# Kernel optimization log

Measured on AMD Instinct MI355X. Metric: run time of the kernel, lower is better.

Reference implementation:

```python
import jax, jax.numpy as jnp
import numpy as np

BN_EPS = 1e-5

def gin_layer(x, src, dst, w1, b1, w2, b2, gamma, beta):
    # GINConv with eps=0: h_i = MLP(x_i + sum_{j->i} x_j)
    agg = jax.ops.segment_sum(x[src], dst, num_segments=x.shape[0])  # [N, D]
    h = x + agg
    h = jnp.maximum(h @ w1 + b1, 0.0) @ w2 + b2
    # BatchNorm (training-mode batch statistics, biased var as in torch)
    mu = jnp.mean(h, axis=0)
    var = jnp.var(h, axis=0)
    h = (h - mu) * jax.lax.rsqrt(var + BN_EPS) * gamma + beta
    return jnp.maximum(h, 0.0)  # ReLU (dropout = identity in eval)

def setup_inputs() -> dict:
    key = jax.random.key(0)
    N, E, G = 20000, 320000, 64
    dims = [128, 128, 256, 512]
    ks = jax.random.split(key, 32)
    inp = {
        "x": jax.random.normal(ks[0], (N, dims[0]), dtype=jnp.float32),
        "edge_index": jax.random.randint(ks[1], (2, E), 0, N, dtype=jnp.int64),
        "batch_idx": jnp.sort(jax.random.randint(ks[2], (N,), 0, G, dtype=jnp.int64)),
    }
    ki = 3
    for li, (di, do) in enumerate(zip(dims[:-1], dims[1:])):
        s = chr(ord('a') + li)
        inp[f"w1{s}"] = jax.random.normal(ks[ki], (di, do), dtype=jnp.float32) * (1.0 / np.sqrt(di)); ki += 1
        inp[f"b1{s}"] = jnp.zeros((do,), dtype=jnp.float32)
        inp[f"w2{s}"] = jax.random.normal(ks[ki], (do, do), dtype=jnp.float32) * (1.0 / np.sqrt(do)); ki += 1
        inp[f"b2{s}"] = jnp.zeros((do,), dtype=jnp.float32)
        inp[f"gn{s}"] = jnp.ones((do,), dtype=jnp.float32)
        inp[f"bn{s}"] = jnp.zeros((do,), dtype=jnp.float32)
    inp["wo"] = jax.random.normal(ks[ki], (dims[-1], 64), dtype=jnp.float32) * (1.0 / np.sqrt(dims[-1]))
    inp["bo"] = jnp.zeros((64,), dtype=jnp.float32)
    return inp

def reference(x, edge_index, batch_idx,
              w1a, b1a, w2a, b2a, gna, bna,
              w1b, b1b, w2b, b2b, gnb, bnb,
              w1c, b1c, w2c, b2c, gnc, bnc,
              wo, bo):
    G = 64
    src, dst = edge_index[0], edge_index[1]
    h = gin_layer(x, src, dst, w1a, b1a, w2a, b2a, gna, bna)
    h = gin_layer(h, src, dst, w1b, b1b, w2b, b2b, gnb, bnb)
    h = gin_layer(h, src, dst, w1c, b1c, w2c, b2c, gnc, bnc)
    # global mean pool over graphs
    sums = jax.ops.segment_sum(h, batch_idx, num_segments=G)  # [G, 512]
    cnts = jax.ops.segment_sum(jnp.ones((h.shape[0],), h.dtype), batch_idx, num_segments=G)
    pooled = sums / jnp.maximum(cnts, 1.0)[:, None]
    # output projection: Linear -> ReLU (dropout identity in eval)
    return jnp.maximum(pooled @ wo + bo, 0.0)
```

## Files before the change

kernel.cpp:

```cpp
#include <hip/hip_runtime.h>

typedef float f32x4 __attribute__((ext_vector_type(4)));
typedef _Float16 f16x2 __attribute__((ext_vector_type(2)));
typedef _Float16 f16x4 __attribute__((ext_vector_type(4)));
typedef _Float16 f16x8 __attribute__((ext_vector_type(8)));

__device__ __forceinline__ void gload_lds16(const _Float16* g, _Float16* l) {
  __builtin_amdgcn_global_load_lds(
      (const __attribute__((address_space(1))) unsigned int*)g,
      (__attribute__((address_space(3))) unsigned int*)l, 16, 0, 0);
}

__global__ __launch_bounds__(256) void hist_kernel(const int* __restrict__ dst,
                                                   int* __restrict__ deg, int E) {
  int e = blockIdx.x * 256 + threadIdx.x;
  if (e < E) atomicAdd(&deg[dst[e]], 1);
}

__global__ __launch_bounds__(1024) void scan_kernel(const int* __restrict__ deg,
                                                    int* __restrict__ rowstart,
                                                    int* __restrict__ cursor, int N) {
  __shared__ int sums[1024];
  const int t = threadIdx.x;
  const int CH = (N + 1023) >> 10;
  int local[32];
  int base = t * CH;
  int s = 0;
  for (int i = 0; i < CH; i++) {
    int idx = base + i;
    int v = (idx < N) ? deg[idx] : 0;
    local[i] = s;
    s += v;
  }
  sums[t] = s;
  __syncthreads();
  for (int off = 1; off < 1024; off <<= 1) {
    int add = (t >= off) ? sums[t - off] : 0;
    __syncthreads();
    sums[t] += add;
    __syncthreads();
  }
  int prefix = sums[t] - s;
  for (int i = 0; i < CH; i++) {
    int idx = base + i;
    if (idx < N) {
      int v = prefix + local[i];
      rowstart[idx] = v;
      cursor[idx] = v;
    }
  }
  if (t == 1023) rowstart[N] = sums[1023];
}

__global__ __launch_bounds__(256) void fill_kernel(const int* __restrict__ src,
                                                   const int* __restrict__ dst,
                                                   int* __restrict__ cursor,
                                                   int* __restrict__ nbr, int E) {
  int e = blockIdx.x * 256 + threadIdx.x;
  if (e >= E) return;
  int pos = atomicAdd(&cursor[dst[e]], 1);
  nbr[pos] = src[e];
}

__global__ __launch_bounds__(256) void xprep_kernel(const float4* __restrict__ in,
                                                    f16x4* __restrict__ out, int n4,
                                                    int* __restrict__ deg, int N,
                                                    float* __restrict__ zbuf, int zn) {
  int i = blockIdx.x * 256 + threadIdx.x;
  if (i < N) deg[i] = 0;
  if (i < zn) zbuf[i] = 0.f;
  if (i >= n4) return;
  float4 v = in[i];
  f16x4 h;
  h[0] = (_Float16)v.x; h[1] = (_Float16)v.y;
  h[2] = (_Float16)v.z; h[3] = (_Float16)v.w;
  out[i] = h;
}

template <int C, bool BNIN>
__global__ __launch_bounds__(256) void gather_agg_kernel(
    const _Float16* __restrict__ x, const int* __restrict__ rowstart,
    const int* __restrict__ nbr, const float* __restrict__ stats,
    const float* __restrict__ gamma, const float* __restrict__ beta,
    _Float16* __restrict__ agg, int N, float invN) {
  constexpr int Din = 64 * C;
  const int wave = threadIdx.x >> 6;
  const int lane = threadIdx.x & 63;
  const int node = blockIdx.x * 4 + wave;
  if (node >= N) return;

  float sc[C], sh[C];
  if constexpr (BNIN) {
#pragma unroll
    for (int j = 0; j < C; j++) {
      int c = lane * C + j;
      float mean = stats[c] * invN;
      float var = stats[Din + c] * invN - mean * mean;
      sc[j] = rsqrtf(var + 1e-5f) * gamma[c];
      sh[j] = beta[c] - mean * sc[j];
    }
  }

#define LOADROW(dstv, rowidx)                                              \
  {                                                                        \
    const _Float16* _p = x + (size_t)(rowidx)*Din + lane * C;              \
    if constexpr (C == 2) {                                                \
      f16x2 _t = *(const f16x2*)_p;                                        \
      dstv[0] = (float)_t[0]; dstv[1] = (float)_t[1];                      \
    } else {                                                               \
      f16x4 _t = *(const f16x4*)_p;                                        \
      dstv[0] = (float)_t[0]; dstv[1] = (float)_t[1];                      \
      dstv[2] = (float)_t[2]; dstv[3] = (float)_t[3];                      \
    }                                                                      \
  }
#define ACCUM(vv)                                                          \
  _Pragma("unroll") for (int j = 0; j < C; j++)                            \
      acc[j] += BNIN ? fmaxf(vv[j] * sc[j] + sh[j], 0.f) : vv[j];

  float acc[C];
  {
    float v[C];
    LOADROW(v, node)
#pragma unroll
    for (int j = 0; j < C; j++)
      acc[j] = BNIN ? fmaxf(v[j] * sc[j] + sh[j], 0.f) : v[j];
  }
  const int rs = rowstart[node], re = rowstart[node + 1];
  int e = rs;
  for (; e + 3 < re; e += 4) {
    int s0 = nbr[e], s1 = nbr[e + 1], s2 = nbr[e + 2], s3 = nbr[e + 3];
    float v0[C], v1[C], v2[C], v3[C];
    LOADROW(v0, s0)
    LOADROW(v1, s1)
    LOADROW(v2, s2)
    LOADROW(v3, s3)
    ACCUM(v0) ACCUM(v1) ACCUM(v2) ACCUM(v3)
  }
  for (; e + 1 < re; e += 2) {
    int s0 = nbr[e], s1 = nbr[e + 1];
    float v0[C], v1[C];
    LOADROW(v0, s0)
    LOADROW(v1, s1)
    ACCUM(v0) ACCUM(v1)
  }
  if (e < re) {
    int s0 = nbr[e];
    float v0[C];
    LOADROW(v0, s0)
    ACCUM(v0)
  }
#undef ACCUM
#undef LOADROW

  _Float16* o = agg + (size_t)node * Din + lane * C;
  if constexpr (C == 2) {
    f16x2 r; r[0] = (_Float16)acc[0]; r[1] = (_Float16)acc[1];
    *(f16x2*)o = r;
  } else {
    f16x4 r;
    r[0] = (_Float16)acc[0]; r[1] = (_Float16)acc[1];
    r[2] = (_Float16)acc[2]; r[3] = (_Float16)acc[3];
    *(f16x4*)o = r;
  }
}

struct WSeg {
  const float* W;
  _Float16* TH;
  int K, N, total;
};
struct WAll { WSeg s[6]; };

__global__ __launch_bounds__(256) void wprep_all_kernel(WAll a) {
  WSeg sg = a.s[blockIdx.y];
  int idx = blockIdx.x * 256 + threadIdx.x;
  if (idx >= sg.total) return;
  int k = idx / sg.N, n = idx - k * sg.N;
  sg.TH[(size_t)n * sg.K + k] = (_Float16)sg.W[idx];
}

template <int RT>
__global__ __launch_bounds__(256, 8) void gemm_mfma_kernel(
    const _Float16* __restrict__ A, const _Float16* __restrict__ BT,
    const float* __restrict__ bias, _Float16* __restrict__ Ch,
    int M, int K, int N, int mblocks, int cbShift,
    int doRelu, float* __restrict__ stats) {
  constexpr int NF = RT / 16;
  constexpr int NFT = 2 * NF;
  constexpr int FPW = NFT / 4;
  __shared__ _Float16 Ah[2][NFT * 512];
  const int bid = blockIdx.x;
  const int xcd = bid & 7;
  const int q = bid >> 3;
  const int r = ((q >> cbShift) << 3) + xcd;
  const int cb = q & ((1 << cbShift) - 1);
  if (r >= mblocks) return;

  const int tid = threadIdx.x;
  const int lane = tid & 63;
  const int w = tid >> 6;
  const int rowBase = r * RT;
  const int colBase = cb * 128 + w * 32;

  f32x4 acc[NF][2] = {};
  const int c0 = colBase + (lane & 15);
  const int kfrag = (lane >> 4) * 8;

  size_t srcOff[FPW];
#pragma unroll
  for (int i = 0; i < FPW; i++) {
    int F = w * FPW + i;
    int ks = F / NF, fi = F % NF;
    int row = rowBase + fi * 16 + (lane & 15);
    row = min(row, M - 1);
    srcOff[i] = (size_t)row * K + ks * 32 + ((lane >> 4) << 3);
  }

#define STAGE(b, t)                                                        \
  {                                                                        \
    _Pragma("unroll") for (int i = 0; i < FPW; i++)                        \
        gload_lds16(A + srcOff[i] + (size_t)(t) * 64,                      \
                    Ah[b] + (w * FPW + i) * 512);                          \
  }

  const int NT = K >> 6;
  STAGE(0, 0)
  __syncthreads();
  int cur = 0;
  for (int t = 0; t < NT; t++) {
    if (t + 1 < NT) {
      if (cur) STAGE(0, t + 1) else STAGE(1, t + 1)
    }
#pragma unroll
    for (int ks = 0; ks < 2; ks++) {
      int kidx = t * 64 + ks * 32 + kfrag;
      f16x8 bh0 = *(const f16x8*)(BT + (size_t)c0 * K + kidx);
      f16x8 bh1 = *(const f16x8*)(BT + (size_t)(c0 + 16) * K + kidx);
#pragma unroll
      for (int fi = 0; fi < NF; fi++) {
        f16x8 ah = *(const f16x8*)(Ah[cur] + (ks * NF + fi) * 512 + lane * 8);
        acc[fi][0] = __builtin_amdgcn_mfma_f32_16x16x32_f16(ah, bh0, acc[fi][0], 0, 0, 0);
        acc[fi][1] = __builtin_amdgcn_mfma_f32_16x16x32_f16(ah, bh1, acc[fi][1], 0, 0, 0);
      }
    }
    __syncthreads();
    cur ^= 1;
  }
#undef STAGE

  const float bias0 = bias[c0], bias1 = bias[c0 + 16];
  float s1[2] = {0.f, 0.f}, s2[2] = {0.f, 0.f};
  const int rbase = rowBase + (lane >> 4) * 4;
#pragma unroll
  for (int fi = 0; fi < NF; fi++) {
#pragma unroll
    for (int j = 0; j < 4; j++) {
      int row = rbase + fi * 16 + j;
      float v0 = acc[fi][0][j] + bias0;
      float v1 = acc[fi][1][j] + bias1;
      if (doRelu) { v0 = fmaxf(v0, 0.f); v1 = fmaxf(v1, 0.f); }
      if (row < M) {
        Ch[(size_t)row * N + c0] = (_Float16)v0;
        Ch[(size_t)row * N + c0 + 16] = (_Float16)v1;
        s1[0] += v0; s2[0] += v0 * v0;
        s1[1] += v1; s2[1] += v1 * v1;
      }
    }
  }
  if (stats) {
#pragma unroll
    for (int off = 16; off < 64; off <<= 1) {
      s1[0] += __shfl_xor(s1[0], off);
      s2[0] += __shfl_xor(s2[0], off);
      s1[1] += __shfl_xor(s1[1], off);
      s2[1] += __shfl_xor(s2[1], off);
    }
    if (lane < 16) {
      atomicAdd(&stats[c0], s1[0]);
      atomicAdd(&stats[N + c0], s2[0]);
      atomicAdd(&stats[c0 + 16], s1[1]);
      atomicAdd(&stats[N + c0 + 16], s2[1]);
    }
  }
}

__global__ __launch_bounds__(256) void bn_pool_kernel(
    const _Float16* __restrict__ h, const float* __restrict__ stats,
    const float* __restrict__ gamma, const float* __restrict__ beta,
    const int* __restrict__ batch, float* __restrict__ pooled, int N, float invN) {
  const int g = blockIdx.x >> 3;
  const int s = blockIdx.x & 7;
  __shared__ int s_lo, s_hi;
  if (threadIdx.x == 0) {
    int lo = 0, hi = N;
    while (lo < hi) { int m = (lo + hi) >> 1; if (batch[m] < g) lo = m + 1; else hi = m; }
    s_lo = lo;
    lo = 0; hi = N;
    while (lo < hi) { int m = (lo + hi) >> 1; if (batch[m] < g + 1) lo = m + 1; else hi = m; }
    s_hi = lo;
  }
  __syncthreads();
  const int lo = s_lo, hi = s_hi, len = hi - lo;
  if (len == 0) return;
  const int per = (len + 7) >> 3;
  const int rs = lo + s * per;
  const int re = min(rs + per, hi);
  if (rs >= re) return;
  const int t = threadIdx.x;
  float scv[2], shv[2];
#pragma unroll
  for (int j = 0; j < 2; j++) {
    int c = 2 * t + j;
    float mean = stats[c] * invN;
    float var = stats[512 + c] * invN - mean * mean;
    scv[j] = rsqrtf(var + 1e-5f) * gamma[c];
    shv[j] = beta[c] - mean * scv[j];
  }
  float ax = 0.f, ay = 0.f;
  for (int r = rs; r < re; r++) {
    f16x2 v = *(const f16x2*)(h + (size_t)r * 512 + 2 * t);
    ax += fmaxf((float)v[0] * scv[0] + shv[0], 0.f);
    ay += fmaxf((float)v[1] * scv[1] + shv[1], 0.f);
  }
  float inv = 1.f / (float)len;
  atomicAdd(&pooled[g * 512 + 2 * t], ax * inv);
  atomicAdd(&pooled[g * 512 + 2 * t + 1], ay * inv);
}

__global__ __launch_bounds__(64) void out_kernel(const float* __restrict__ pooled,
                                                 const float* __restrict__ wo,
                                                 const float* __restrict__ bo,
                                                 float* __restrict__ out) {
  int g = blockIdx.x, o = threadIdx.x;
  float acc = bo[o];
  for (int c = 0; c < 512; c++) acc += pooled[g * 512 + c] * wo[c * 64 + o];
  out[g * 64 + o] = fmaxf(acc, 0.f);
}

extern "C" void kernel_launch(void* const* d_in, const int* in_sizes, int n_in,
                              void* d_out, int out_size, void* d_ws, size_t ws_size,
                              hipStream_t stream) {
  const float* x0 = (const float*)d_in[0];
  const int* ei = (const int*)d_in[1];
  const int* batch = (const int*)d_in[2];
  const int N = in_sizes[0] / 128;
  const int E = in_sizes[1] / 2;
  const int* src = ei;
  const int* dst = ei + E;
  const float* W[3][6];
  for (int li = 0; li < 3; li++)
    for (int k = 0; k < 6; k++) W[li][k] = (const float*)d_in[3 + li * 6 + k];
  const float* wo = (const float*)d_in[21];
  const float* bo = (const float*)d_in[22];
  float* out = (float*)d_out;

  float* stats3 = (float*)d_ws;
  float* pooled = stats3 + 3 * 1024;
  int* deg = (int*)(pooled + 64 * 512);
  int* rowstart = deg + N;
  int* cursor = rowstart + N + 1;
  int* nbr = cursor + N;
  uintptr_t wp = (uintptr_t)(nbr + E);
  wp = (wp + 15) & ~(uintptr_t)15;
  _Float16* aggh = (_Float16*)wp;
  _Float16* h1h = aggh + (size_t)N * 256;
  _Float16* h2h = h1h + (size_t)N * 512;
  _Float16* x0h = h2h + (size_t)N * 512;
  _Float16* wbuf = x0h + (size_t)N * 128;

  const int dins[3] = {128, 128, 256};
  const int douts[3] = {128, 256, 512};

  _Float16* WT[3][2];
  {
    _Float16* p = wbuf;
    for (int li = 0; li < 3; li++) {
      WT[li][0] = p; p += (size_t)dins[li] * douts[li];
      WT[li][1] = p; p += (size_t)douts[li] * douts[li];
    }
  }
  {
    WAll wa;
    int maxTotal = 0;
    for (int li = 0; li < 3; li++) {
      int e1 = dins[li] * douts[li];
      int e2 = douts[li] * douts[li];
      wa.s[li * 2 + 0] = WSeg{W[li][0], WT[li][0], dins[li], douts[li], e1};
      wa.s[li * 2 + 1] = WSeg{W[li][2], WT[li][1], douts[li], douts[li], e2};
      maxTotal = max(maxTotal, max(e1, e2));
    }
    dim3 g((maxTotal + 255) / 256, 6);
    wprep_all_kernel<<<g, 256, 0, stream>>>(wa);
  }

  {
    int n4 = N * 32;
    int zn = 3 * 1024 + 64 * 512;
    xprep_kernel<<<(n4 + 255) / 256, 256, 0, stream>>>(
        (const float4*)x0, (f16x4*)x0h, n4, deg, N, stats3, zn);
  }

  hist_kernel<<<(E + 255) / 256, 256, 0, stream>>>(dst, deg, E);
  scan_kernel<<<1, 1024, 0, stream>>>(deg, rowstart, cursor, N);
  fill_kernel<<<(E + 255) / 256, 256, 0, stream>>>(src, dst, cursor, nbr, E);

  const int mb64 = (N + 63) / 64;
  const int mb64_8 = ((mb64 + 7) / 8) * 8;
  const int mb32 = (N + 31) / 32;
  const int mb32_8 = ((mb32 + 7) / 8) * 8;
  const int gblocks = (N + 3) / 4;
  const float invN = 1.0f / N;

  for (int li = 0; li < 3; li++) {
    int Din = dins[li], Dout = douts[li];
    float* stats = stats3 + li * 1024;
    if (li == 0)
      gather_agg_kernel<2, false><<<gblocks, 256, 0, stream>>>(
          x0h, rowstart, nbr, nullptr, nullptr, nullptr, aggh, N, invN);
    else if (li == 1)
      gather_agg_kernel<2, true><<<gblocks, 256, 0, stream>>>(
          h2h, rowstart, nbr, stats3 + 0 * 1024, W[0][4], W[0][5], aggh, N, invN);
    else
      gather_agg_kernel<4, true><<<gblocks, 256, 0, stream>>>(
          h2h, rowstart, nbr, stats3 + 1 * 1024, W[1][4], W[1][5], aggh, N, invN);

    if (Dout == 128) {
      gemm_mfma_kernel<32><<<mb32_8, 256, 0, stream>>>(aggh, WT[li][0], W[li][1], h1h,
                                                       N, Din, Dout, mb32, 0, 1, nullptr);
      gemm_mfma_kernel<32><<<mb32_8, 256, 0, stream>>>(h1h, WT[li][1], W[li][3], h2h,
                                                       N, Dout, Dout, mb32, 0, 0, stats);
    } else {
      int cbShift = (Dout == 256) ? 1 : 2;
      int nblocks = mb64_8 << cbShift;
      gemm_mfma_kernel<64><<<nblocks, 256, 0, stream>>>(aggh, WT[li][0], W[li][1], h1h,
                                                        N, Din, Dout, mb64, cbShift, 1, nullptr);
      gemm_mfma_kernel<64><<<nblocks, 256, 0, stream>>>(h1h, WT[li][1], W[li][3], h2h,
                                                        N, Dout, Dout, mb64, cbShift, 0, stats);
    }
    if (li == 2) {
      bn_pool_kernel<<<64 * 8, 256, 0, stream>>>(
          h2h, stats3 + 2 * 1024, W[2][4], W[2][5], batch, pooled, N, invN);
    }
  }
  out_kernel<<<64, 64, 0, stream>>>(pooled, wo, bo, out);
}
```

Baseline: 290.4 us.

## Triple-buffer GEMM A-tile LDS staging with prefetch distance two

The MFMA GEMM moves from a double-buffered to a triple-buffered LDS ring for A tiles, prefetching two K-tiles ahead. It uses hand-placed s_waitcnt, raw s_barrier and sched_barrier in place of __syncthreads, and issues the B-fragment global loads before the prefetch so they overlap. The goal is to hide global-to-LDS latency and drop one full barrier wait per iteration. In exchange it uses more LDS and lowers the launch-bounds occupancy hint from 8 to 4 blocks. It also relies on implicit vmcnt ordering before each loop barrier, which risks a race if the DMA loads have not landed.

```diff
diff --git a/kernel.cpp b/kernel.cpp
--- a/kernel.cpp
+++ b/kernel.cpp
@@ -180,7 +180,7 @@
 }
 
 template <int RT>
-__global__ __launch_bounds__(256, 8) void gemm_mfma_kernel(
+__global__ __launch_bounds__(256, 4) void gemm_mfma_kernel(
     const _Float16* __restrict__ A, const _Float16* __restrict__ BT,
     const float* __restrict__ bias, _Float16* __restrict__ Ch,
     int M, int K, int N, int mblocks, int cbShift,
@@ -188,7 +188,7 @@
   constexpr int NF = RT / 16;
   constexpr int NFT = 2 * NF;
   constexpr int FPW = NFT / 4;
-  __shared__ _Float16 Ah[2][NFT * 512];
+  __shared__ _Float16 Ah[3][NFT * 512];
   const int bid = blockIdx.x;
   const int xcd = bid & 7;
   const int q = bid >> 3;
@@ -220,31 +220,52 @@
   {                                                                        \
     _Pragma("unroll") for (int i = 0; i < FPW; i++)                        \
         gload_lds16(A + srcOff[i] + (size_t)(t) * 64,                      \
-                    Ah[b] + (w * FPW + i) * 512);                          \
+                    &Ah[b][(w * FPW + i) * 512]);                          \
   }
 
   const int NT = K >> 6;
   STAGE(0, 0)
-  __syncthreads();
+  if (NT > 1) {
+    STAGE(1, 1)
+    if constexpr (FPW == 2)
+      asm volatile("s_waitcnt vmcnt(2)" ::: "memory");
+    else
+      asm volatile("s_waitcnt vmcnt(1)" ::: "memory");
+  } else {
+    asm volatile("s_waitcnt vmcnt(0)" ::: "memory");
+  }
+  __builtin_amdgcn_s_barrier();
+  __builtin_amdgcn_sched_barrier(0);
+
   int cur = 0;
   for (int t = 0; t < NT; t++) {
-    if (t + 1 < NT) {
-      if (cur) STAGE(0, t + 1) else STAGE(1, t + 1)
-    }
+    f16x8 bh[2][2];
 #pragma unroll
     for (int ks = 0; ks < 2; ks++) {
       int kidx = t * 64 + ks * 32 + kfrag;
-      f16x8 bh0 = *(const f16x8*)(BT + (size_t)c0 * K + kidx);
-      f16x8 bh1 = *(const f16x8*)(BT + (size_t)(c0 + 16) * K + kidx);
+      bh[ks][0] = *(const f16x8*)(BT + (size_t)c0 * K + kidx);
+      bh[ks][1] = *(const f16x8*)(BT + (size_t)(c0 + 16) * K + kidx);
+    }
+    __builtin_amdgcn_sched_barrier(0);
+    if (t + 2 < NT) {
+      int b2 = (cur >= 1) ? cur - 1 : 2;
+      STAGE(b2, t + 2)
+    }
+    __builtin_amdgcn_sched_barrier(0);
+#pragma unroll
+    for (int ks = 0; ks < 2; ks++) {
 #pragma unroll
       for (int fi = 0; fi < NF; fi++) {
-        f16x8 ah = *(const f16x8*)(Ah[cur] + (ks * NF + fi) * 512 + lane * 8);
-        acc[fi][0] = __builtin_amdgcn_mfma_f32_16x16x32_f16(ah, bh0, acc[fi][0], 0, 0, 0);
-        acc[fi][1] = __builtin_amdgcn_mfma_f32_16x16x32_f16(ah, bh1, acc[fi][1], 0, 0, 0);
+        f16x8 ah = *(const f16x8*)(&Ah[cur][(ks * NF + fi) * 512 + lane * 8]);
+        acc[fi][0] = __builtin_amdgcn_mfma_f32_16x16x32_f16(ah, bh[ks][0], acc[fi][0], 0, 0, 0);
+        acc[fi][1] = __builtin_amdgcn_mfma_f32_16x16x32_f16(ah, bh[ks][1], acc[fi][1], 0, 0, 0);
       }
     }
-    __syncthreads();
-    cur ^= 1;
+    if (t + 1 < NT) {
+      __builtin_amdgcn_s_barrier();
+      __builtin_amdgcn_sched_barrier(0);
+    }
+    cur = (cur == 2) ? 0 : cur + 1;
   }
 #undef STAGE
 
```

Result: no change. 290.1 us (-0.1%).
